# Kernel optimization log

Hardware: AMD Instinct MI355X
Metric: run time of the kernel (lower is better)

## Reference

```python
import jax, jax.numpy as jnp
import numpy as np

B, E, C = 256, 512, 256          # batch, entity_size, entity_embedding_size
AR, H256, H32 = 1024, 256, 32
NUM_ACTIONS, MAX_UNIT_TYPE = 564, 256
MAX_SELECTED = 64
TEMPERATURE = 1.0                # is_sl_training=True -> temperature forced to 1.0


def setup_inputs() -> dict:
    key = jax.random.key(0)
    ks = jax.random.split(key, 20)
    s = 0.02
    inp = {
        "autoregressive_embedding": jax.random.normal(ks[0], (B, AR), jnp.float32),
        "action_type": jax.random.randint(ks[1], (B, 1), 0, NUM_ACTIONS, jnp.int64),
        "entity_embeddings": jax.random.normal(ks[2], (B, E, C), jnp.float32),
        # func_embed Dense(max_unit_type -> 256)
        "Wf": jax.random.normal(ks[3], (MAX_UNIT_TYPE, H256)) * s,
        "bf": jnp.zeros((H256,)),
        # conv_1 Conv1D(kernel_size=1): C -> 32
        "Wk": jax.random.normal(ks[4], (C, H32)) * s,
        "bk": jnp.zeros((H32,)),
        # fc_1 Dense(AR -> 256)
        "W1": jax.random.normal(ks[5], (AR, H256)) * s,
        "b1": jnp.zeros((H256,)),
        # fc_2 Dense(256 -> 32)
        "W2": jax.random.normal(ks[6], (H256, H32)) * s,
        "b2": jnp.zeros((H32,)),
        # small_lstm: input 32 -> hidden 32, keras gate order (i, f, g, o)
        "Wx": jax.random.normal(ks[7], (H32, 4 * H32)) * s,
        "Wh": jax.random.normal(ks[8], (H32, 4 * H32)) * s,
        "bl": jnp.zeros((4 * H32,)),
        # project Dense(32 -> AR)
        "Wp": jax.random.normal(ks[9], (H32, AR)) * s,
        "bp": jnp.zeros((AR,)),
        # stand-ins for utils.action_can_apply_to_entity_types_mask / action_involve_selecting_units_mask
        "unit_mask_table": (jax.random.uniform(ks[10], (NUM_ACTIONS, MAX_UNIT_TYPE)) < 0.5).astype(jnp.float32),
        "select_table": (jax.random.uniform(ks[11], (NUM_ACTIONS,)) < 0.5).astype(jnp.float32),
    }
    return inp


def _lstm_step(x, h, c, Wx, Wh, bl):
    z = x @ Wx + h @ Wh + bl                       # [B, 4H]
    i, f, g, o = jnp.split(z, 4, axis=-1)
    i, f, o = jax.nn.sigmoid(i), jax.nn.sigmoid(f), jax.nn.sigmoid(o)
    c = f * c + i * jnp.tanh(g)
    h = o * jnp.tanh(c)
    return h, c


def reference(autoregressive_embedding, action_type, entity_embeddings,
              Wf, bf, Wk, bk, W1, b1, W2, b2, Wx, Wh, bl, Wp, bp,
              unit_mask_table, select_table):
    a = action_type[:, 0]                                          # [B]
    unit_types_one_hot = unit_mask_table[a]                        # [B, max_unit_type]
    the_func_embed = jax.nn.relu(unit_types_one_hot @ Wf + bf)     # [B, 256]
    key_proj = jnp.einsum('bec,ch->beh', entity_embeddings, Wk) + bk  # [B, E, 32]

    sample_key = jax.random.key(42)
    h0 = jnp.zeros((B, H32), entity_embeddings.dtype)
    c0 = jnp.zeros((B, H32), entity_embeddings.dtype)
    mask0 = jnp.ones((B, E), entity_embeddings.dtype)

    def body(carry, _):
        ar, mask, h, c, rng = carry
        x = ar @ W1 + b1                                           # fc_1
        z2 = jax.nn.relu(the_func_embed + x) @ W2 + b2             # fc_2, [B, 32]
        h, c = _lstm_step(z2, h, c, Wx, Wh, bl)                    # single LSTM step
        query = h                                                  # [B, 32]
        y = jnp.einsum('beh,bh->be', key_proj, query)              # attention scores
        y2 = y * jax.lax.stop_gradient(mask)
        entity_logits = y2 / TEMPERATURE                           # [B, E]
        entity_probs = jax.nn.softmax(entity_logits, axis=-1)
        rng, sub = jax.random.split(rng)
        # tf.random.categorical treats its input as logits -> Gumbel-argmax over entity_probs
        gumbel = -jnp.log(-jnp.log(jax.random.uniform(sub, (B, E), minval=1e-20, maxval=1.0)))
        entity_id = jnp.argmax(entity_probs + gumbel, axis=-1)     # [B]
        mask = mask.at[jnp.arange(B), entity_id].set(0.0)
        one_hot = jax.nn.one_hot(entity_id, E, dtype=key_proj.dtype)
        out = jnp.einsum('be,beh->bh', one_hot, key_proj)          # [B, 32]
        out = out - jnp.mean(one_hot, axis=-1, keepdims=True)
        ar = ar + (out @ Wp + bp)
        return (ar, mask, h, c, rng), (entity_logits, entity_id)

    (ar, _, _, _, _), (logits_seq, units_seq) = jax.lax.scan(
        body, (autoregressive_embedding, mask0, h0, c0, sample_key), None, length=MAX_SELECTED)

    units_logits = jnp.transpose(logits_seq, (1, 0, 2))            # [B, S, E]
    units = jnp.transpose(units_seq, (1, 0))[:, :, None]           # [B, S, 1]

    select = select_table[a][:, None]                              # [B, 1]
    units_logits = units_logits * select[:, :, None]
    units = units * select[:, :, None].astype(units.dtype)
    ar = ar * select
    return units_logits, units, ar
```

## Files before the change

### kernel.cpp

```cpp
#include <hip/hip_runtime.h>


#define JAX_PARTITIONABLE 1

typedef unsigned int u32;
typedef _Float16 half2v __attribute__((ext_vector_type(2)));

#define NB 256
#define NE 512
#define NT 64
#define KPW 40

#define OFF_UNITS 8388608
#define OFF_AR    8404992

#define WS_WQ   0
#define WS_CV   8192
#define WS_XF0  8448
#define WS_WK2  73984

struct U2 { u32 a, b; };

__host__ __device__ constexpr u32 rotl32(u32 x, int r) {
  return (x << r) | (x >> (32 - r));
}

__host__ __device__ constexpr U2 tf2x32(u32 k0, u32 k1, u32 x0, u32 x1) {
  u32 ks2 = k0 ^ k1 ^ 0x1BD11BDAu;
  x0 += k0; x1 += k1;
  x0 += x1; x1 = rotl32(x1, 13); x1 ^= x0;
  x0 += x1; x1 = rotl32(x1, 15); x1 ^= x0;
  x0 += x1; x1 = rotl32(x1, 26); x1 ^= x0;
  x0 += x1; x1 = rotl32(x1, 6);  x1 ^= x0;
  x0 += k1; x1 += ks2 + 1u;
  x0 += x1; x1 = rotl32(x1, 17); x1 ^= x0;
  x0 += x1; x1 = rotl32(x1, 29); x1 ^= x0;
  x0 += x1; x1 = rotl32(x1, 16); x1 ^= x0;
  x0 += x1; x1 = rotl32(x1, 24); x1 ^= x0;
  x0 += ks2; x1 += k0 + 2u;
  x0 += x1; x1 = rotl32(x1, 13); x1 ^= x0;
  x0 += x1; x1 = rotl32(x1, 15); x1 ^= x0;
  x0 += x1; x1 = rotl32(x1, 26); x1 ^= x0;
  x0 += x1; x1 = rotl32(x1, 6);  x1 ^= x0;
  x0 += k0; x1 += k1 + 3u;
  x0 += x1; x1 = rotl32(x1, 17); x1 ^= x0;
  x0 += x1; x1 = rotl32(x1, 29); x1 ^= x0;
  x0 += x1; x1 = rotl32(x1, 16); x1 ^= x0;
  x0 += x1; x1 = rotl32(x1, 24); x1 ^= x0;
  x0 += k1; x1 += ks2 + 4u;
  x0 += x1; x1 = rotl32(x1, 13); x1 ^= x0;
  x0 += x1; x1 = rotl32(x1, 15); x1 ^= x0;
  x0 += x1; x1 = rotl32(x1, 26); x1 ^= x0;
  x0 += x1; x1 = rotl32(x1, 6);  x1 ^= x0;
  x0 += ks2; x1 += k0 + 5u;
  return U2{x0, x1};
}

struct KeyTab { u32 s0[NT]; u32 s1[NT]; };

__host__ __device__ constexpr KeyTab make_tab() {
  KeyTab t{};
  u32 k0 = 0u, k1 = 42u;
  for (int i = 0; i < NT; ++i) {
#if JAX_PARTITIONABLE
    U2 nk = tf2x32(k0, k1, 0u, 0u);
    U2 sb = tf2x32(k0, k1, 0u, 1u);
#else
    U2 r02 = tf2x32(k0, k1, 0u, 2u);
    U2 r13 = tf2x32(k0, k1, 1u, 3u);
    U2 nk{r02.a, r13.a};
    U2 sb{r02.b, r13.b};
#endif
    t.s0[i] = sb.a; t.s1[i] = sb.b;
    k0 = nk.a; k1 = nk.b;
  }
  return t;
}

__constant__ KeyTab SUBTAB = make_tab();

__device__ __forceinline__ float gumbel_draw(u32 k0, u32 k1, u32 jf) {
#if JAX_PARTITIONABLE
  U2 v = tf2x32(k0, k1, 0u, jf);
  u32 bits = v.a ^ v.b;
#else
  u32 bits;
  if (jf < 65536u) { U2 v = tf2x32(k0, k1, jf, jf + 65536u); bits = v.a; }
  else             { U2 v = tf2x32(k0, k1, jf - 65536u, jf); bits = v.b; }
#endif
  float f = __uint_as_float((bits >> 9) | 0x3f800000u) - 1.0f;
  float u = f + 1e-20f;
  u = fmaxf(u, 1e-20f);
  return -logf(-logf(u));
}

__device__ __forceinline__ float fdot2f(half2v a, half2v b, float c) {
#if __has_builtin(__builtin_amdgcn_fdot2)
  return __builtin_amdgcn_fdot2(a, b, c, false);
#else
  return c + (float)a.x * (float)b.x + (float)a.y * (float)b.y;
#endif
}

__global__ __launch_bounds__(512) void suh_prep(
    const float* __restrict__ ar0, const int* __restrict__ act,
    const float* __restrict__ Wf, const float* __restrict__ bfv,
    const float* __restrict__ W1, const float* __restrict__ b1,
    const float* __restrict__ Wp, const float* __restrict__ bp,
    const float* __restrict__ Wk, const float* __restrict__ umt,
    float* __restrict__ ws)
{
  __shared__ float lvec[1024];
  __shared__ float red2[512];
  __shared__ float feL[256];
  __shared__ float lum[256];
  const int t = threadIdx.x;
  const int bid = blockIdx.x;

  if (bid == NB + 33) return;

  if (bid == NB + 33 - 0 || bid == 289) {
    half2v* wkp = (half2v*)(ws + WS_WK2);
    #pragma unroll
    for (int i = 0; i < 8; ++i) {
      const int p = t * 8 + i;
      const int c2 = p >> 5, h = p & 31;
      half2v v = { (_Float16)Wk[c2 * 64 + h], (_Float16)Wk[c2 * 64 + 32 + h] };
      wkp[p] = v;
    }
    return;
  }

  const int o = t & 255, hf = t >> 8;
  const float* src;
  if (bid < NB) src = ar0 + bid * 1024;
  else if (bid < NB + 32) src = Wp + (bid - NB) * 1024;
  else src = bp;

  for (int i = t; i < 1024; i += 512) lvec[i] = src[i];
  if (bid < NB && t < 256) lum[t] = umt[act[bid] * 256 + t];
  __syncthreads();

  float p = 0.0f;
  const int kb = hf * 512;
  #pragma unroll 16
  for (int k = 0; k < 512; ++k) p = fmaf(lvec[kb + k], W1[(kb + k) * 256 + o], p);
  red2[hf * 256 + o] = p;
  if (bid < NB && hf == 1) {
    float fe = bfv[o];
    #pragma unroll 8
    for (int k = 0; k < 256; ++k) fe = fmaf(lum[k], Wf[k * 256 + o], fe);
    feL[o] = fmaxf(fe, 0.0f);
  }
  __syncthreads();

  if (t < 256) {
    const float s = red2[t] + red2[256 + t];
    if (bid < NB)            ws[WS_XF0 + bid * 256 + t] = s + b1[t] + feL[t];
    else if (bid < NB + 32)  ws[WS_WQ + (bid - NB) * 256 + t] = s;
    else                     ws[WS_CV + t] = s;
  }
}

__global__ __launch_bounds__(512, 2) void suh_main(
    const float* __restrict__ ar0, const int* __restrict__ act,
    const float* __restrict__ emb, const float* __restrict__ bk,
    const float* __restrict__ W2, const float* __restrict__ b2,
    const float* __restrict__ Wx, const float* __restrict__ Wh,
    const float* __restrict__ bl, const float* __restrict__ Wp,
    const float* __restrict__ bp, const float* __restrict__ selt,
    const float* __restrict__ ws, float* __restrict__ outp)
{
  const int b = blockIdx.x;
  const int t = threadIdx.x;
  const float sel = selt[act[b]];
  float* outL = outp;
  float* outU = outp + OFF_UNITS;
  float* outA = outp + OFF_AR;

  if (sel == 0.0f) {
    float4 z4 = {0.0f, 0.0f, 0.0f, 0.0f};
    float4* pl = (float4*)(outL + (size_t)b * 32768);
    for (int i = t; i < 8192; i += 512) pl[i] = z4;
    if (t < 16) ((float4*)(outU + b * 64))[t] = z4;
    if (t < 256) ((float4*)(outA + b * 1024))[t] = z4;
    return;
  }

  __shared__ __align__(16) _Float16 kph[NE * KPW];
  __shared__ float wq[8192];
  __shared__ __align__(16) float xf[256];
  __shared__ float maskv[NE];
  __shared__ float red[512];
  __shared__ float cvs[256];
  __shared__ float gumL[64];
  __shared__ float sacc[32];
  __shared__ __align__(16) half2v h2b[16];
  __shared__ float wsum[8];
  __shared__ float wargv[8];
  __shared__ int   wargi[8];

  const int hh = t & 31, kc = t >> 5;
  float w2r[16];
  #pragma unroll
  for (int i = 0; i < 16; ++i) w2r[i] = W2[(kc * 16 + i) * 32 + hh];

  float wx0[32], wx1[32], wh0[32], wh1[32];
  float blv0 = 0.0f, blv1 = 0.0f, b2v = 0.0f;
  float hv = 0.0f, cv = 0.0f;
  if (t < 64) {
    const int c0 = t, c1 = 64 + t;
    #pragma unroll
    for (int r = 0; r < 32; ++r) {
      wx0[r] = Wx[r * 128 + c0]; wx1[r] = Wx[r * 128 + c1];
      wh0[r] = Wh[r * 128 + c0]; wh1[r] = Wh[r * 128 + c1];
    }
    blv0 = bl[c0]; blv1 = bl[c1]; b2v = b2[t & 31];
  }

  if (t < 256) {
    xf[t] = ws[WS_XF0 + b * 256 + t];
    cvs[t] = ws[WS_CV + t];
    #pragma unroll
    for (int i = 0; i < 8; ++i) wq[i * 1024 + (t & 255) * 4 + (i & 0)] = 0.0f;
  }
  {
    const float4* s4 = (const float4*)(ws + WS_WQ);
    float4* d4 = (float4*)wq;
    for (int i = t; i < 2048; i += 512) d4[i] = s4[i];
  }
  if (t < 32) sacc[t] = 0.0f;
  maskv[t] = 1.0f;

  {
    float acc[32];
    #pragma unroll
    for (int h = 0; h < 32; ++h) acc[h] = bk[h];
    const float4* erow = (const float4*)(emb + (size_t)b * (NE * 256) + (size_t)t * 256);
    const half2v* wkg = (const half2v*)(ws + WS_WK2);
    for (int c4 = 0; c4 < 64; ++c4) {
      float4 ev = erow[c4];
      half2v e01 = { (_Float16)ev.x, (_Float16)ev.y };
      half2v e23 = { (_Float16)ev.z, (_Float16)ev.w };
      const half2v* w0 = wkg + (2 * c4) * 32;
      const half2v* w1 = w0 + 32;
      #pragma unroll
      for (int h = 0; h < 32; ++h) {
        acc[h] = fdot2f(e01, w0[h], acc[h]);
        acc[h] = fdot2f(e23, w1[h], acc[h]);
      }
    }
    half2v* kr = (half2v*)(kph + t * KPW);
    #pragma unroll
    for (int j = 0; j < 16; ++j) {
      half2v v = { (_Float16)acc[2 * j], (_Float16)acc[2 * j + 1] };
      kr[j] = v;
    }
  }
  __syncthreads();

  const u32 jf_own = (u32)(b * 512 + t);

  for (int step = 0; step < NT; ++step) {
    const u32 sk0 = SUBTAB.s0[step], sk1 = SUBTAB.s1[step];
    float gum = 0.0f;
    if (t >= 64) gum = gumbel_draw(sk0, sk1, jf_own);
    if (t >= 64 && t < 128) gumL[t - 64] = gumbel_draw(sk0, sk1, jf_own - 64u);

    {
      float pa = 0.0f;
      const float* xk = &xf[kc * 16];
      #pragma unroll
      for (int i = 0; i < 16; ++i) pa = fmaf(fmaxf(xk[i], 0.0f), w2r[i], pa);
      red[kc * 32 + hh] = pa;
    }
    __syncthreads();

    if (t < 64) {
      const int h = t & 31, half = t >> 5;
      float z = 0.0f;
      #pragma unroll
      for (int i = 0; i < 8; ++i) z += red[(half * 8 + i) * 32 + h];
      z += __shfl_xor(z, 32);
      const float z2v = z + b2v;

      float g0 = blv0, g1 = blv1;
      #pragma unroll
      for (int r = 0; r < 32; ++r) {
        const float zr = __shfl(z2v, r);
        const float hr = __shfl(hv, r);
        g0 = fmaf(zr, wx0[r], g0); g0 = fmaf(hr, wh0[r], g0);
        g1 = fmaf(zr, wx1[r], g1); g1 = fmaf(hr, wh1[r], g1);
      }
      const float zf = __shfl_xor(g0, 32);
      const float zo = __shfl_xor(g1, 32);
      if (t < 32) {
        const float si = 1.0f / (1.0f + expf(-g0));
        const float sf = 1.0f / (1.0f + expf(-zf));
        const float so = 1.0f / (1.0f + expf(-zo));
        cv = sf * cv + si * tanhf(g1);
        hv = so * tanhf(cv);
      }
      const float ha = __shfl(hv, 2 * (t & 31));
      const float hb = __shfl(hv, 2 * (t & 31) + 1);
      if (t < 16) { half2v v = { (_Float16)ha, (_Float16)hb }; h2b[t] = v; }
    }
    __syncthreads();

    if (t < 64) gum = gumL[t];
    float yv = 0.0f;
    {
      const half2v* k2 = (const half2v*)(kph + t * KPW);
      #pragma unroll
      for (int j = 0; j < 16; ++j) yv = fdot2f(k2[j], h2b[j], yv);
    }
    const float y2 = yv * maskv[t];
    outL[(size_t)b * 32768 + step * 512 + t] = y2;
    const float ev = expf(y2);
    float sv = ev;
    #pragma unroll
    for (int s = 1; s < 64; s <<= 1) sv += __shfl_xor(sv, s);
    if ((t & 63) == 0) wsum[t >> 6] = sv;
    __syncthreads();

    float Z = wsum[0];
    #pragma unroll
    for (int i = 1; i < 8; ++i) Z += wsum[i];
    float val = ev / Z + gum;
    int idx = t;
    #pragma unroll
    for (int s = 1; s < 64; s <<= 1) {
      const float vo = __shfl_xor(val, s);
      const int io = __shfl_xor(idx, s);
      if (vo > val || (vo == val && io < idx)) { val = vo; idx = io; }
    }
    if ((t & 63) == 0) { wargv[t >> 6] = val; wargi[t >> 6] = idx; }
    __syncthreads();

    float bvv = wargv[0]; int id = wargi[0];
    #pragma unroll
    for (int i = 1; i < 8; ++i) {
      if (wargv[i] > bvv || (wargv[i] == bvv && wargi[i] < id)) { bvv = wargv[i]; id = wargi[i]; }
    }

    if (t == 0) { maskv[id] = 0.0f; outU[b * 64 + step] = (float)id; }
    if (t < 32) sacc[t] += (float)kph[id * KPW + t] - 0.001953125f;
    if (t < 256) {
      const half2v* kid = (const half2v*)(kph + id * KPW);
      float dx = cvs[t];
      #pragma unroll
      for (int j = 0; j < 16; ++j) {
        half2v kj = kid[j];
        dx = fmaf((float)kj.x - 0.001953125f, wq[(2 * j) * 256 + t], dx);
        dx = fmaf((float)kj.y - 0.001953125f, wq[(2 * j + 1) * 256 + t], dx);
      }
      xf[t] += dx;
    }
    __syncthreads();
  }

  for (int j = t; j < 1024; j += 512) {
    float acc2 = ar0[b * 1024 + j] + 64.0f * bp[j];
    #pragma unroll 8
    for (int r = 0; r < 32; ++r) acc2 = fmaf(sacc[r], Wp[r * 1024 + j], acc2);
    outA[b * 1024 + j] = acc2;
  }
}

extern "C" void kernel_launch(void* const* d_in, const int* in_sizes, int n_in,
                              void* d_out, int out_size, void* d_ws, size_t ws_size,
                              hipStream_t stream)
{
  (void)in_sizes; (void)n_in; (void)out_size; (void)ws_size;
  const float* ar0 = (const float*)d_in[0];
  const int*   act = (const int*)d_in[1];
  const float* emb = (const float*)d_in[2];
  const float* Wf  = (const float*)d_in[3];
  const float* bfv = (const float*)d_in[4];
  const float* Wk  = (const float*)d_in[5];
  const float* bk  = (const float*)d_in[6];
  const float* W1  = (const float*)d_in[7];
  const float* b1  = (const float*)d_in[8];
  const float* W2  = (const float*)d_in[9];
  const float* b2  = (const float*)d_in[10];
  const float* Wx  = (const float*)d_in[11];
  const float* Wh  = (const float*)d_in[12];
  const float* bl  = (const float*)d_in[13];
  const float* Wp  = (const float*)d_in[14];
  const float* bp  = (const float*)d_in[15];
  const float* umt = (const float*)d_in[16];
  const float* selt = (const float*)d_in[17];
  float* ws = (float*)d_ws;
  float* outp = (float*)d_out;

  suh_prep<<<dim3(290), dim3(512), 0, stream>>>(ar0, act, Wf, bfv, W1, b1, Wp, bp, Wk, umt, ws);
  suh_main<<<dim3(256), dim3(512), 0, stream>>>(ar0, act, emb, bk, W2, b2, Wx, Wh,
                                                bl, Wp, bp, selt, ws, outp);
}
```

Measured before the change: 558.9 us.

## Precompute Gumbel noise in separate kernel, transpose key layout, use fast math

Adds a kernel that fills all per-step Gumbel noise into workspace (when the workspace is large enough), so the main loop reads it instead of running Threefry and two logs per element on the serial critical path. The key projection is stored transposed as half2 planes, which avoids bank conflicts. The LSTM weights move from registers to packed half2 in LDS, and launch bounds change to one block per SM. Fast __expf/__logf intrinsics and an LDS-only waitcnt barrier replace the full-precision calls and __syncthreads. In exchange it writes and reads a 32 MB buffer, and LSTM weights in half precision plus the fast intrinsics change numerics slightly.

Result: faster. 540.0 us (-3.4%).

```diff
diff --git a/kernel.cpp b/kernel.cpp
--- a/kernel.cpp
+++ b/kernel.cpp
@@ -9,7 +9,6 @@
 #define NB 256
 #define NE 512
 #define NT 64
-#define KPW 40
 
 #define OFF_UNITS 8388608
 #define OFF_AR    8404992
@@ -18,6 +17,9 @@
 #define WS_CV   8192
 #define WS_XF0  8448
 #define WS_WK2  73984
+#define WS_GU   78080
+
+#define BARL() asm volatile("s_waitcnt lgkmcnt(0)\n\ts_barrier" ::: "memory")
 
 struct U2 { u32 a, b; };
 
@@ -91,7 +93,7 @@
   float f = __uint_as_float((bits >> 9) | 0x3f800000u) - 1.0f;
   float u = f + 1e-20f;
   u = fmaxf(u, 1e-20f);
-  return -logf(-logf(u));
+  return -__logf(-__logf(u));
 }
 
 __device__ __forceinline__ float fdot2f(half2v a, half2v b, float c) {
@@ -100,6 +102,18 @@
 #else
   return c + (float)a.x * (float)b.x + (float)a.y * (float)b.y;
 #endif
+}
+
+__global__ __launch_bounds__(512) void suh_gum(
+    const int* __restrict__ act, const float* __restrict__ selt,
+    float* __restrict__ gws)
+{
+  const u32 blk = blockIdx.x;
+  const int b = (int)(blk >> 6), step = (int)(blk & 63u);
+  if (selt[act[b]] == 0.0f) return;
+  const int e = threadIdx.x;
+  gws[((size_t)blk << 9) | (u32)e] =
+      gumbel_draw(SUBTAB.s0[step], SUBTAB.s1[step], (u32)(b * 512 + e));
 }
 
 __global__ __launch_bounds__(512) void suh_prep(
@@ -117,9 +131,7 @@
   const int t = threadIdx.x;
   const int bid = blockIdx.x;
 
-  if (bid == NB + 33) return;
-
-  if (bid == NB + 33 - 0 || bid == 289) {
+  if (bid >= 289) {
     half2v* wkp = (half2v*)(ws + WS_WK2);
     #pragma unroll
     for (int i = 0; i < 8; ++i) {
@@ -162,14 +174,15 @@
   }
 }
 
-__global__ __launch_bounds__(512, 2) void suh_main(
+__global__ __launch_bounds__(512, 1) void suh_main(
     const float* __restrict__ ar0, const int* __restrict__ act,
     const float* __restrict__ emb, const float* __restrict__ bk,
     const float* __restrict__ W2, const float* __restrict__ b2,
     const float* __restrict__ Wx, const float* __restrict__ Wh,
     const float* __restrict__ bl, const float* __restrict__ Wp,
     const float* __restrict__ bp, const float* __restrict__ selt,
-    const float* __restrict__ ws, float* __restrict__ outp)
+    const float* __restrict__ ws, const float* __restrict__ gws,
+    const int use_pre, float* __restrict__ outp)
 {
   const int b = blockIdx.x;
   const int t = threadIdx.x;
@@ -187,15 +200,15 @@
     return;
   }
 
-  __shared__ __align__(16) _Float16 kph[NE * KPW];
-  __shared__ float wq[8192];
-  __shared__ __align__(16) float xf[256];
+  __shared__ half2v kpT[16][NE];
+  __shared__ float wq[32][256];
+  __shared__ half2v whx[4096];
+  __shared__ float xf[256];
   __shared__ float maskv[NE];
   __shared__ float red[512];
   __shared__ float cvs[256];
-  __shared__ float gumL[64];
   __shared__ float sacc[32];
-  __shared__ __align__(16) half2v h2b[16];
+  __shared__ half2v h2b[16];
   __shared__ float wsum[8];
   __shared__ float wargv[8];
   __shared__ int   wargi[8];
@@ -205,30 +218,21 @@
   #pragma unroll
   for (int i = 0; i < 16; ++i) w2r[i] = W2[(kc * 16 + i) * 32 + hh];
 
-  float wx0[32], wx1[32], wh0[32], wh1[32];
   float blv0 = 0.0f, blv1 = 0.0f, b2v = 0.0f;
   float hv = 0.0f, cv = 0.0f;
-  if (t < 64) {
-    const int c0 = t, c1 = 64 + t;
-    #pragma unroll
-    for (int r = 0; r < 32; ++r) {
-      wx0[r] = Wx[r * 128 + c0]; wx1[r] = Wx[r * 128 + c1];
-      wh0[r] = Wh[r * 128 + c0]; wh1[r] = Wh[r * 128 + c1];
-    }
-    blv0 = bl[c0]; blv1 = bl[c1]; b2v = b2[t & 31];
-  }
-
-  if (t < 256) {
-    xf[t] = ws[WS_XF0 + b * 256 + t];
-    cvs[t] = ws[WS_CV + t];
-    #pragma unroll
-    for (int i = 0; i < 8; ++i) wq[i * 1024 + (t & 255) * 4 + (i & 0)] = 0.0f;
+  if (t < 64) { blv0 = bl[t]; blv1 = bl[64 + t]; b2v = b2[t & 31]; }
+
+  for (int i = t; i < 4096; i += 512) {
+    const int r = i >> 7, g = i & 127;
+    half2v v = { (_Float16)Wx[r * 128 + g], (_Float16)Wh[r * 128 + g] };
+    whx[i] = v;
   }
   {
     const float4* s4 = (const float4*)(ws + WS_WQ);
-    float4* d4 = (float4*)wq;
+    float4* d4 = (float4*)&wq[0][0];
     for (int i = t; i < 2048; i += 512) d4[i] = s4[i];
   }
+  if (t < 256) { xf[t] = ws[WS_XF0 + b * 256 + t]; cvs[t] = ws[WS_CV + t]; }
   if (t < 32) sacc[t] = 0.0f;
   maskv[t] = 1.0f;
 
@@ -250,22 +254,20 @@
         acc[h] = fdot2f(e23, w1[h], acc[h]);
       }
     }
-    half2v* kr = (half2v*)(kph + t * KPW);
     #pragma unroll
     for (int j = 0; j < 16; ++j) {
       half2v v = { (_Float16)acc[2 * j], (_Float16)acc[2 * j + 1] };
-      kr[j] = v;
+      kpT[j][t] = v;
     }
   }
   __syncthreads();
 
-  const u32 jf_own = (u32)(b * 512 + t);
+  const size_t gbase = (size_t)b * 64 * 512 + t;
 
   for (int step = 0; step < NT; ++step) {
-    const u32 sk0 = SUBTAB.s0[step], sk1 = SUBTAB.s1[step];
-    float gum = 0.0f;
-    if (t >= 64) gum = gumbel_draw(sk0, sk1, jf_own);
-    if (t >= 64 && t < 128) gumL[t - 64] = gumbel_draw(sk0, sk1, jf_own - 64u);
+    float gum;
+    if (use_pre) gum = gws[gbase + (size_t)step * 512];
+    else gum = gumbel_draw(SUBTAB.s0[step], SUBTAB.s1[step], (u32)(b * 512 + t));
 
     {
       float pa = 0.0f;
@@ -274,7 +276,7 @@
       for (int i = 0; i < 16; ++i) pa = fmaf(fmaxf(xk[i], 0.0f), w2r[i], pa);
       red[kc * 32 + hh] = pa;
     }
-    __syncthreads();
+    BARL();
 
     if (t < 64) {
       const int h = t & 31, half = t >> 5;
@@ -289,15 +291,17 @@
       for (int r = 0; r < 32; ++r) {
         const float zr = __shfl(z2v, r);
         const float hr = __shfl(hv, r);
-        g0 = fmaf(zr, wx0[r], g0); g0 = fmaf(hr, wh0[r], g0);
-        g1 = fmaf(zr, wx1[r], g1); g1 = fmaf(hr, wh1[r], g1);
+        half2v p0 = whx[r * 128 + t];
+        half2v p1 = whx[r * 128 + 64 + t];
+        g0 = fmaf(zr, (float)p0.x, g0); g0 = fmaf(hr, (float)p0.y, g0);
+        g1 = fmaf(zr, (float)p1.x, g1); g1 = fmaf(hr, (float)p1.y, g1);
       }
       const float zf = __shfl_xor(g0, 32);
       const float zo = __shfl_xor(g1, 32);
       if (t < 32) {
-        const float si = 1.0f / (1.0f + expf(-g0));
-        const float sf = 1.0f / (1.0f + expf(-zf));
-        const float so = 1.0f / (1.0f + expf(-zo));
+        const float si = 1.0f / (1.0f + __expf(-g0));
+        const float sf = 1.0f / (1.0f + __expf(-zf));
+        const float so = 1.0f / (1.0f + __expf(-zo));
         cv = sf * cv + si * tanhf(g1);
         hv = so * tanhf(cv);
       }
@@ -305,23 +309,24 @@
       const float hb = __shfl(hv, 2 * (t & 31) + 1);
       if (t < 16) { half2v v = { (_Float16)ha, (_Float16)hb }; h2b[t] = v; }
     }
-    __syncthreads();
-
-    if (t < 64) gum = gumL[t];
-    float yv = 0.0f;
-    {
-      const half2v* k2 = (const half2v*)(kph + t * KPW);
-      #pragma unroll
-      for (int j = 0; j < 16; ++j) yv = fdot2f(k2[j], h2b[j], yv);
-    }
-    const float y2 = yv * maskv[t];
+    BARL();
+
+    float a0 = 0.0f, a1 = 0.0f, a2 = 0.0f, a3 = 0.0f;
+    #pragma unroll
+    for (int j = 0; j < 16; j += 4) {
+      a0 = fdot2f(kpT[j][t],     h2b[j],     a0);
+      a1 = fdot2f(kpT[j + 1][t], h2b[j + 1], a1);
+      a2 = fdot2f(kpT[j + 2][t], h2b[j + 2], a2);
+      a3 = fdot2f(kpT[j + 3][t], h2b[j + 3], a3);
+    }
+    const float y2 = ((a0 + a1) + (a2 + a3)) * maskv[t];
     outL[(size_t)b * 32768 + step * 512 + t] = y2;
-    const float ev = expf(y2);
+    const float ev = __expf(y2);
     float sv = ev;
     #pragma unroll
     for (int s = 1; s < 64; s <<= 1) sv += __shfl_xor(sv, s);
     if ((t & 63) == 0) wsum[t >> 6] = sv;
-    __syncthreads();
+    BARL();
 
     float Z = wsum[0];
     #pragma unroll
@@ -335,7 +340,7 @@
       if (vo > val || (vo == val && io < idx)) { val = vo; idx = io; }
     }
     if ((t & 63) == 0) { wargv[t >> 6] = val; wargi[t >> 6] = idx; }
-    __syncthreads();
+    BARL();
 
     float bvv = wargv[0]; int id = wargi[0];
     #pragma unroll
@@ -344,19 +349,22 @@
     }
 
     if (t == 0) { maskv[id] = 0.0f; outU[b * 64 + step] = (float)id; }
-    if (t < 32) sacc[t] += (float)kph[id * KPW + t] - 0.001953125f;
+    if (t < 32) {
+      half2v kj = kpT[t >> 1][id];
+      const float kv = (t & 1) ? (float)kj.y : (float)kj.x;
+      sacc[t] += kv - 0.001953125f;
+    }
     if (t < 256) {
-      const half2v* kid = (const half2v*)(kph + id * KPW);
       float dx = cvs[t];
       #pragma unroll
       for (int j = 0; j < 16; ++j) {
-        half2v kj = kid[j];
-        dx = fmaf((float)kj.x - 0.001953125f, wq[(2 * j) * 256 + t], dx);
-        dx = fmaf((float)kj.y - 0.001953125f, wq[(2 * j + 1) * 256 + t], dx);
+        half2v kj = kpT[j][id];
+        dx = fmaf((float)kj.x - 0.001953125f, wq[2 * j][t], dx);
+        dx = fmaf((float)kj.y - 0.001953125f, wq[2 * j + 1][t], dx);
       }
       xf[t] += dx;
     }
-    __syncthreads();
+    BARL();
   }
 
   for (int j = t; j < 1024; j += 512) {
@@ -371,7 +379,7 @@
                               void* d_out, int out_size, void* d_ws, size_t ws_size,
                               hipStream_t stream)
 {
-  (void)in_sizes; (void)n_in; (void)out_size; (void)ws_size;
+  (void)in_sizes; (void)n_in; (void)out_size;
   const float* ar0 = (const float*)d_in[0];
   const int*   act = (const int*)d_in[1];
   const float* emb = (const float*)d_in[2];
@@ -393,7 +401,13 @@
   float* ws = (float*)d_ws;
   float* outp = (float*)d_out;
 
+  const size_t need = (size_t)(WS_GU + 8388608) * sizeof(float);
+  const int use_pre = (ws_size >= need) ? 1 : 0;
+
   suh_prep<<<dim3(290), dim3(512), 0, stream>>>(ar0, act, Wf, bfv, W1, b1, Wp, bp, Wk, umt, ws);
+  if (use_pre)
+    suh_gum<<<dim3(16384), dim3(512), 0, stream>>>(act, selt, ws + WS_GU);
   suh_main<<<dim3(256), dim3(512), 0, stream>>>(ar0, act, emb, bk, W2, b2, Wx, Wh,
-                                                bl, Wp, bp, selt, ws, outp);
-}
+                                                bl, Wp, bp, selt, ws, ws + WS_GU,
+                                                use_pre, outp);
+}
```
